# Optimization experiments

Measured on AMD Instinct MI355X. Metric: run time of the kernel, lower is better.

## Reference

```python
import jax, jax.numpy as jnp
import numpy as np

N_NODES = 100000

def _gcn_norm(edge_index, num_nodes):
    # add self-loops, compute symmetric normalization coeffs per edge
    loops = jnp.arange(num_nodes, dtype=edge_index.dtype)
    src = jnp.concatenate([edge_index[0], loops])
    dst = jnp.concatenate([edge_index[1], loops])
    deg = jax.ops.segment_sum(jnp.ones_like(dst, dtype=jnp.float32), dst,
                              num_segments=num_nodes)
    dinv = jnp.where(deg > 0, jax.lax.rsqrt(deg), 0.0)
    norm = dinv[src] * dinv[dst]  # [E + N]
    return src, dst, norm

def _gcn_conv(x, W, b, src, dst, norm, num_nodes):
    h = x @ W                              # [N, out] transform first (PyG order)
    msg = h[src] * norm[:, None]           # gather + scale
    out = jax.ops.segment_sum(msg, dst, num_segments=num_nodes)  # scatter-add
    return out + b

def setup_inputs() -> dict:
    key = jax.random.key(0)
    k1, k2, k3, k4 = jax.random.split(key, 4)
    F_in, H, C = 128, 64, 40
    x = jax.random.normal(k1, (N_NODES, F_in), dtype=jnp.float32)
    edge_index = jax.random.randint(k2, (2, 1600000), 0, N_NODES, dtype=jnp.int64)
    W1 = jax.random.normal(k3, (F_in, H), dtype=jnp.float32) / np.sqrt(F_in)
    b1 = jnp.zeros((H,), dtype=jnp.float32)
    W2 = jax.random.normal(k4, (H, C), dtype=jnp.float32) / np.sqrt(H)
    b2 = jnp.zeros((C,), dtype=jnp.float32)
    return {"x": x, "edge_index": edge_index, "W1": W1, "b1": b1, "W2": W2, "b2": b2}

def reference(x, edge_index, W1, b1, W2, b2):
    num_nodes = x.shape[0]
    src, dst, norm = _gcn_norm(edge_index, num_nodes)
    h = _gcn_conv(x, W1, b1, src, dst, norm, num_nodes)
    h = jax.nn.relu(h)
    # dropout is identity in eval mode (training=False)
    h = _gcn_conv(h, W2, b2, src, dst, norm, num_nodes)
    return jax.nn.log_softmax(h, axis=1)
```

## Files before the change

kernel.cpp:

```cpp
#include <hip/hip_runtime.h>
#include <math.h>

#define NPB 256
#define BSH 8
#define MAXNB 400
#define BIN_CHUNK 8192
#define HIST_CHUNK 16384

typedef __attribute__((ext_vector_type(8))) short bf16x8;
typedef __attribute__((ext_vector_type(4))) float f32x4;
typedef __attribute__((ext_vector_type(2))) float f32x2;

__device__ __forceinline__ unsigned short f2bf(float f){
  unsigned int u = __float_as_uint(f);
  unsigned int r = (u + 0x7FFFu + ((u >> 16) & 1u)) >> 16;
  return (unsigned short)r;
}
__device__ __forceinline__ float bf2f(unsigned int b){
  return __uint_as_float(b << 16);
}

__device__ __forceinline__ bf16x8 cvt8(float4 a, float4 b){
  union { unsigned u[4]; bf16x8 v; } r;
  asm("v_cvt_pk_bf16_f32 %0, %1, %2" : "=v"(r.u[0]) : "v"(a.x), "v"(a.y));
  asm("v_cvt_pk_bf16_f32 %0, %1, %2" : "=v"(r.u[1]) : "v"(a.z), "v"(a.w));
  asm("v_cvt_pk_bf16_f32 %0, %1, %2" : "=v"(r.u[2]) : "v"(b.x), "v"(b.y));
  asm("v_cvt_pk_bf16_f32 %0, %1, %2" : "=v"(r.u[3]) : "v"(b.z), "v"(b.w));
  return r.v;
}


__global__ void k_zero(int* __restrict__ p, int n){
  int i = blockIdx.x*256 + threadIdx.x;
  if(i < n) p[i] = 0;
}

__global__ __launch_bounds__(256) void k_bhist(const int* __restrict__ dst, int E,
                                               int* __restrict__ bcnt, int NB){
  __shared__ int l[MAXNB];
  int t = threadIdx.x;
  int base = blockIdx.x*HIST_CHUNK;
  int end = base + HIST_CHUNK; if(end > E) end = E;
  for(int b = t; b < NB; b += 256) l[b] = 0;
  __syncthreads();
  for(int i = base + t; i < end; i += 256) atomicAdd(&l[dst[i] >> BSH], 1);
  __syncthreads();
  for(int b = t; b < NB; b += 256){ int c = l[b]; if(c) atomicAdd(&bcnt[b], c); }
}

__global__ void k_bscan(const int* __restrict__ bcnt, int* __restrict__ bofs,
                        int* __restrict__ bcur, int NB, int E){
  __shared__ int sh[1024];
  int t = threadIdx.x;
  int c0 = (2*t   < NB) ? bcnt[2*t]   : 0;
  int c1 = (2*t+1 < NB) ? bcnt[2*t+1] : 0;
  sh[t] = c0 + c1; __syncthreads();
  for(int off = 1; off < 1024; off <<= 1){
    int v = (t >= off) ? sh[t - off] : 0;
    __syncthreads();
    sh[t] += v;
    __syncthreads();
  }
  int pairEx = sh[t] - (c0 + c1);
  if(2*t   < NB){ bofs[2*t]   = pairEx;      bcur[2*t]   = pairEx; }
  if(2*t+1 < NB){ bofs[2*t+1] = pairEx + c0; bcur[2*t+1] = pairEx + c0; }
  if(t == 0) bofs[NB] = E;
}

__global__ __launch_bounds__(256) void k_binpass(const int* __restrict__ src,
                          const int* __restrict__ dst, int E,
                          int* __restrict__ bcur, unsigned int* __restrict__ binned, int NB){
  __shared__ int lcnt[MAXNB];
  __shared__ int lpos[MAXNB];
  int t = threadIdx.x;
  int base = blockIdx.x * BIN_CHUNK;
  int end = base + BIN_CHUNK; if(end > E) end = E;
  for(int b = t; b < NB; b += 256) lcnt[b] = 0;
  __syncthreads();
  for(int i = base + t; i < end; i += 256)
    atomicAdd(&lcnt[dst[i] >> BSH], 1);
  __syncthreads();
  for(int b = t; b < NB; b += 256){
    int c = lcnt[b];
    lpos[b] = c ? atomicAdd(&bcur[b], c) : 0;
  }
  __syncthreads();
  for(int i = base + t; i < end; i += 256){
    int d = dst[i];
    int b = d >> BSH;
    unsigned int rec = (unsigned int)src[i] | ((unsigned int)(d & (NPB-1)) << 17);
    int p = atomicAdd(&lpos[b], 1);
    binned[p] = rec;
  }
}

__global__ __launch_bounds__(256) void k_bscatter(const unsigned int* __restrict__ binned,
     const int* __restrict__ bofs, int* __restrict__ csr, int* __restrict__ row_ofs,
     float* __restrict__ dinv, int N, int E, int NB){
  __shared__ int lcnt[NPB];
  __shared__ int lofs[NPB];
  __shared__ int lcur[NPB];
  __shared__ int wsum[4];
  int b = blockIdx.x, t = threadIdx.x;
  int beg = bofs[b], end = bofs[b+1];
  lcnt[t] = 0;
  __syncthreads();
  for(int i = beg + t; i < end; i += 256) atomicAdd(&lcnt[binned[i] >> 17], 1);
  __syncthreads();
  int c = lcnt[t];
  int lane = t & 63, wid = t >> 6;
  int v = c;
  #pragma unroll
  for(int off = 1; off < 64; off <<= 1){
    int nv = __shfl_up(v, off, 64);
    if(lane >= off) v += nv;
  }
  if(lane == 63) wsum[wid] = v;
  __syncthreads();
  int wpre = 0;
  #pragma unroll
  for(int k2 = 0; k2 < 4; k2++) if(k2 < wid) wpre += wsum[k2];
  int ex = wpre + v - c;
  lofs[t] = beg + ex; lcur[t] = 0;
  int node = (b << BSH) + t;
  if(node < N){
    row_ofs[node] = beg + ex;
    dinv[node] = rsqrtf((float)(c + 1));
  }
  __syncthreads();
  for(int i = beg + t; i < end; i += 256){
    unsigned int rec = binned[i];
    int dl = rec >> 17;
    int pos = lofs[dl] + atomicAdd(&lcur[dl], 1);
    csr[pos] = (int)(rec & 0x1FFFFu);
  }
  if(b == NB-1 && t == 0) row_ofs[N] = E;
}

__global__ void k_wprep(const float* __restrict__ W1, unsigned short* __restrict__ w1t){
  int t = threadIdx.x;
  for(int i = t; i < 8192; i += 256){
    int k = i >> 6, f = i & 63;
    w1t[f*128 + k] = f2bf(W1[i]);
  }
}

__global__ __launch_bounds__(256) void k_gemm1(const float* __restrict__ x,
                        const unsigned short* __restrict__ w1t,
                        const float* __restrict__ dinv, unsigned int* __restrict__ g1, int n){
  __shared__ unsigned short wt[64*136];
  int tid = threadIdx.x;
  int nodeBase = blockIdx.x*128;
  for(int i = tid; i < 1024; i += 256){
    int f = i >> 4, seg = i & 15;
    uint4 v = *(const uint4*)&w1t[f*128 + seg*8];
    *(uint4*)&wt[f*136 + seg*8] = v;
  }
  __syncthreads();

  int w = tid >> 6, lane = tid & 63;
  int ml = lane & 15, q = lane >> 4;
  int n0 = nodeBase + w*32 + ml;
  int n1 = n0 + 16;
  bool vn0 = n0 < n, vn1 = n1 < n;
  const float* px0 = x + (size_t)n0*128 + q*8;
  const float* px1 = x + (size_t)n1*128 + q*8;
  const float4 z4 = make_float4(0.f,0.f,0.f,0.f);

  f32x4 a00 = {0.f,0.f,0.f,0.f}, a01 = {0.f,0.f,0.f,0.f},
        a02 = {0.f,0.f,0.f,0.f}, a03 = {0.f,0.f,0.f,0.f};
  f32x4 a10 = {0.f,0.f,0.f,0.f}, a11 = {0.f,0.f,0.f,0.f},
        a12 = {0.f,0.f,0.f,0.f}, a13 = {0.f,0.f,0.f,0.f};
  const unsigned short* arow = &wt[ml*136 + q*8];
  #pragma unroll
  for(int s = 0; s < 4; s++){
    float4 xa0 = vn0 ? *(const float4*)(px0 + s*32)     : z4;
    float4 xb0 = vn0 ? *(const float4*)(px0 + s*32 + 4) : z4;
    float4 xa1 = vn1 ? *(const float4*)(px1 + s*32)     : z4;
    float4 xb1 = vn1 ? *(const float4*)(px1 + s*32 + 4) : z4;
    bf16x8 bb0 = cvt8(xa0, xb0);
    bf16x8 bb1 = cvt8(xa1, xb1);
    bf16x8 a0 = *(const bf16x8*)(arow +    0 + s*32);
    bf16x8 a1 = *(const bf16x8*)(arow + 2176 + s*32);
    bf16x8 a2 = *(const bf16x8*)(arow + 4352 + s*32);
    bf16x8 a3 = *(const bf16x8*)(arow + 6528 + s*32);
    a00 = __builtin_amdgcn_mfma_f32_16x16x32_bf16(a0, bb0, a00, 0, 0, 0);
    a01 = __builtin_amdgcn_mfma_f32_16x16x32_bf16(a1, bb0, a01, 0, 0, 0);
    a02 = __builtin_amdgcn_mfma_f32_16x16x32_bf16(a2, bb0, a02, 0, 0, 0);
    a03 = __builtin_amdgcn_mfma_f32_16x16x32_bf16(a3, bb0, a03, 0, 0, 0);
    a10 = __builtin_amdgcn_mfma_f32_16x16x32_bf16(a0, bb1, a10, 0, 0, 0);
    a11 = __builtin_amdgcn_mfma_f32_16x16x32_bf16(a1, bb1, a11, 0, 0, 0);
    a12 = __builtin_amdgcn_mfma_f32_16x16x32_bf16(a2, bb1, a12, 0, 0, 0);
    a13 = __builtin_amdgcn_mfma_f32_16x16x32_bf16(a3, bb1, a13, 0, 0, 0);
  }
  if(vn0){
    float dv = dinv[n0];
    unsigned base16 = ((unsigned)n0 << 4) + q;
    int p;
    p = __builtin_amdgcn_cvt_pk_fp8_f32(a00[0]*dv, a00[1]*dv, 0, false);
    p = __builtin_amdgcn_cvt_pk_fp8_f32(a00[2]*dv, a00[3]*dv, p, true);
    g1[base16 +  0] = (unsigned)p;
    p = __builtin_amdgcn_cvt_pk_fp8_f32(a01[0]*dv, a01[1]*dv, 0, false);
    p = __builtin_amdgcn_cvt_pk_fp8_f32(a01[2]*dv, a01[3]*dv, p, true);
    g1[base16 +  4] = (unsigned)p;
    p = __builtin_amdgcn_cvt_pk_fp8_f32(a02[0]*dv, a02[1]*dv, 0, false);
    p = __builtin_amdgcn_cvt_pk_fp8_f32(a02[2]*dv, a02[3]*dv, p, true);
    g1[base16 +  8] = (unsigned)p;
    p = __builtin_amdgcn_cvt_pk_fp8_f32(a03[0]*dv, a03[1]*dv, 0, false);
    p = __builtin_amdgcn_cvt_pk_fp8_f32(a03[2]*dv, a03[3]*dv, p, true);
    g1[base16 + 12] = (unsigned)p;
  }
  if(vn1){
    float dv = dinv[n1];
    unsigned base16 = ((unsigned)n1 << 4) + q;
    int p;
    p = __builtin_amdgcn_cvt_pk_fp8_f32(a10[0]*dv, a10[1]*dv, 0, false);
    p = __builtin_amdgcn_cvt_pk_fp8_f32(a10[2]*dv, a10[3]*dv, p, true);
    g1[base16 +  0] = (unsigned)p;
    p = __builtin_amdgcn_cvt_pk_fp8_f32(a11[0]*dv, a11[1]*dv, 0, false);
    p = __builtin_amdgcn_cvt_pk_fp8_f32(a11[2]*dv, a11[3]*dv, p, true);
    g1[base16 +  4] = (unsigned)p;
    p = __builtin_amdgcn_cvt_pk_fp8_f32(a12[0]*dv, a12[1]*dv, 0, false);
    p = __builtin_amdgcn_cvt_pk_fp8_f32(a12[2]*dv, a12[3]*dv, p, true);
    g1[base16 +  8] = (unsigned)p;
    p = __builtin_amdgcn_cvt_pk_fp8_f32(a13[0]*dv, a13[1]*dv, 0, false);
    p = __builtin_amdgcn_cvt_pk_fp8_f32(a13[2]*dv, a13[3]*dv, p, true);
    g1[base16 + 12] = (unsigned)p;
  }
}

__global__ __launch_bounds__(256) void k_agg1(const unsigned* __restrict__ g1,
    const int* __restrict__ row_ofs, const int* __restrict__ csr,
    const float* __restrict__ dinv, const float* __restrict__ b1,
    unsigned short* __restrict__ u, int N){
  int t = threadIdx.x;
  int lane = t & 63;
  int f = lane & 15;
  int bq = (lane & 48) << 2;
  int node = blockIdx.x*16 + (t >> 4);
  if(node >= N) return;
  int beg = row_ofs[node], end = row_ofs[node+1];
  unsigned v = g1[((unsigned)node << 4) + f];
  f32x2 s01 = __builtin_amdgcn_cvt_pk_f32_fp8(v, false);
  f32x2 s23 = __builtin_amdgcn_cvt_pk_f32_fp8(v, true);
  for(int e = beg; e < end; e += 16){
    int rem = end - e; if(rem > 16) rem = 16;
    int idxv = (f < rem) ? csr[e + f] : 0;
    int j = 0;
    for(; j + 4 <= rem; j += 4){
      int r0 = __builtin_amdgcn_ds_bpermute(bq + ((j+0) << 2), idxv);
      int r1 = __builtin_amdgcn_ds_bpermute(bq + ((j+1) << 2), idxv);
      int r2 = __builtin_amdgcn_ds_bpermute(bq + ((j+2) << 2), idxv);
      int r3 = __builtin_amdgcn_ds_bpermute(bq + ((j+3) << 2), idxv);
      unsigned v0 = g1[((unsigned)r0 << 4) + f];
      unsigned v1 = g1[((unsigned)r1 << 4) + f];
      unsigned v2 = g1[((unsigned)r2 << 4) + f];
      unsigned v3 = g1[((unsigned)r3 << 4) + f];
      s01 += __builtin_amdgcn_cvt_pk_f32_fp8(v0, false);
      s23 += __builtin_amdgcn_cvt_pk_f32_fp8(v0, true);
      s01 += __builtin_amdgcn_cvt_pk_f32_fp8(v1, false);
      s23 += __builtin_amdgcn_cvt_pk_f32_fp8(v1, true);
      s01 += __builtin_amdgcn_cvt_pk_f32_fp8(v2, false);
      s23 += __builtin_amdgcn_cvt_pk_f32_fp8(v2, true);
      s01 += __builtin_amdgcn_cvt_pk_f32_fp8(v3, false);
      s23 += __builtin_amdgcn_cvt_pk_f32_fp8(v3, true);
    }
    for(; j < rem; j++){
      int r0 = __builtin_amdgcn_ds_bpermute(bq + (j << 2), idxv);
      unsigned v0 = g1[((unsigned)r0 << 4) + f];
      s01 += __builtin_amdgcn_cvt_pk_f32_fp8(v0, false);
      s23 += __builtin_amdgcn_cvt_pk_f32_fp8(v0, true);
    }
  }
  float dv = dinv[node];
  float4 bb = ((const float4*)b1)[f];
  float h0 = fmaxf(fmaf(dv, s01.x, bb.x), 0.f);
  float h1 = fmaxf(fmaf(dv, s01.y, bb.y), 0.f);
  float h2 = fmaxf(fmaf(dv, s23.x, bb.z), 0.f);
  float h3 = fmaxf(fmaf(dv, s23.y, bb.w), 0.f);
  unsigned p0 = (unsigned)f2bf(dv*h0) | ((unsigned)f2bf(dv*h1) << 16);
  unsigned p1 = (unsigned)f2bf(dv*h2) | ((unsigned)f2bf(dv*h3) << 16);
  ((uint2*)u)[((unsigned)node << 4) + f] = make_uint2(p0, p1);
}

__global__ __launch_bounds__(320) void k_gemm2(const unsigned short* __restrict__ u,
                        const float* __restrict__ W2, unsigned char* __restrict__ g2, int n){
  __shared__ float hs[64*65];
  __shared__ float ws[64*40];
  int t = threadIdx.x;
  int nodeBase = blockIdx.x*64;
  for(int i = t; i < 2560; i += 320) ws[i] = W2[i];
  for(int i = t; i < 512; i += 320){
    int row = i >> 3, seg = i & 7;
    uint4 v = make_uint4(0,0,0,0);
    if(nodeBase + row < n) v = *(const uint4*)&u[(size_t)(nodeBase + row)*64 + seg*8];
    float* dp = &hs[row*65 + seg*8];
    dp[0]=bf2f(v.x&0xFFFFu); dp[1]=bf2f(v.x>>16);
    dp[2]=bf2f(v.y&0xFFFFu); dp[3]=bf2f(v.y>>16);
    dp[4]=bf2f(v.z&0xFFFFu); dp[5]=bf2f(v.z>>16);
    dp[6]=bf2f(v.w&0xFFFFu); dp[7]=bf2f(v.w>>16);
  }
  __syncthreads();
  int seg = t >> 6, lane = t & 63;
  float acc[8] = {0.f,0.f,0.f,0.f,0.f,0.f,0.f,0.f};
  const float* hrow = &hs[lane*65];
  const float* wcol = &ws[seg*8];
  #pragma unroll 4
  for(int k = 0; k < 64; k++){
    float a = hrow[k];
    #pragma unroll
    for(int j = 0; j < 8; j++) acc[j] = fmaf(a, wcol[k*40 + j], acc[j]);
  }
  int node = nodeBase + lane;
  if(node < n){
    int p0 = __builtin_amdgcn_cvt_pk_fp8_f32(acc[0], acc[1], 0, false);
    p0     = __builtin_amdgcn_cvt_pk_fp8_f32(acc[2], acc[3], p0, true);
    int p1 = __builtin_amdgcn_cvt_pk_fp8_f32(acc[4], acc[5], 0, false);
    p1     = __builtin_amdgcn_cvt_pk_fp8_f32(acc[6], acc[7], p1, true);
    *(uint2*)&g2[(size_t)node*40 + seg*8] = make_uint2((unsigned)p0, (unsigned)p1);
  }
}

__global__ __launch_bounds__(256) void k_agg2(const unsigned char* __restrict__ g2,
     const int* __restrict__ row_ofs, const int* __restrict__ csr,
     const float* __restrict__ dinv, const float* __restrict__ b2,
     float* __restrict__ out, int N){
  int t = threadIdx.x;
  int lane = t & 63;
  int f = lane & 15;
  int fc = (f < 10) ? f : 0;
  int bq = (lane & 48) << 2;
  int node = blockIdx.x*16 + (t >> 4);
  if(node >= N) return;
  int beg = row_ofs[node], end = row_ofs[node+1];
  const unsigned* gd = (const unsigned*)g2;
  unsigned v = gd[(unsigned)node*10u + fc];
  f32x2 s01 = __builtin_amdgcn_cvt_pk_f32_fp8(v, false);
  f32x2 s23 = __builtin_amdgcn_cvt_pk_f32_fp8(v, true);
  for(int e = beg; e < end; e += 16){
    int rem = end - e; if(rem > 16) rem = 16;
    int idxv = (f < rem) ? csr[e + f] : 0;
    int j = 0;
    for(; j + 4 <= rem; j += 4){
      int r0 = __builtin_amdgcn_ds_bpermute(bq + ((j+0) << 2), idxv);
      int r1 = __builtin_amdgcn_ds_bpermute(bq + ((j+1) << 2), idxv);
      int r2 = __builtin_amdgcn_ds_bpermute(bq + ((j+2) << 2), idxv);
      int r3 = __builtin_amdgcn_ds_bpermute(bq + ((j+3) << 2), idxv);
      unsigned v0 = gd[(unsigned)r0*10u + fc];
      unsigned v1 = gd[(unsigned)r1*10u + fc];
      unsigned v2 = gd[(unsigned)r2*10u + fc];
      unsigned v3 = gd[(unsigned)r3*10u + fc];
      s01 += __builtin_amdgcn_cvt_pk_f32_fp8(v0, false);
      s23 += __builtin_amdgcn_cvt_pk_f32_fp8(v0, true);
      s01 += __builtin_amdgcn_cvt_pk_f32_fp8(v1, false);
      s23 += __builtin_amdgcn_cvt_pk_f32_fp8(v1, true);
      s01 += __builtin_amdgcn_cvt_pk_f32_fp8(v2, false);
      s23 += __builtin_amdgcn_cvt_pk_f32_fp8(v2, true);
      s01 += __builtin_amdgcn_cvt_pk_f32_fp8(v3, false);
      s23 += __builtin_amdgcn_cvt_pk_f32_fp8(v3, true);
    }
    for(; j < rem; j++){
      int r0 = __builtin_amdgcn_ds_bpermute(bq + (j << 2), idxv);
      unsigned v0 = gd[(unsigned)r0*10u + fc];
      s01 += __builtin_amdgcn_cvt_pk_f32_fp8(v0, false);
      s23 += __builtin_amdgcn_cvt_pk_f32_fp8(v0, true);
    }
  }
  float dv = dinv[node];
  float4 bb = ((const float4*)b2)[fc];
  float l0 = fmaf(dv, s01.x, bb.x);
  float l1 = fmaf(dv, s01.y, bb.y);
  float l2 = fmaf(dv, s23.x, bb.z);
  float l3 = fmaf(dv, s23.y, bb.w);
  bool valid = (f < 10);
  float m = valid ? fmaxf(fmaxf(l0,l1), fmaxf(l2,l3)) : -INFINITY;
  m = fmaxf(m, __shfl_xor(m,1,64)); m = fmaxf(m, __shfl_xor(m,2,64));
  m = fmaxf(m, __shfl_xor(m,4,64)); m = fmaxf(m, __shfl_xor(m,8,64));
  float ex = valid ? (expf(l0-m)+expf(l1-m)) + (expf(l2-m)+expf(l3-m)) : 0.f;
  ex += __shfl_xor(ex,1,64); ex += __shfl_xor(ex,2,64);
  ex += __shfl_xor(ex,4,64); ex += __shfl_xor(ex,8,64);
  float ll = logf(ex);
  if(valid){
    ((float4*)out)[(unsigned)node*10u + f] = make_float4(l0-m-ll, l1-m-ll, l2-m-ll, l3-m-ll);
  }
}


extern "C" void kernel_launch(void* const* d_in, const int* in_sizes, int n_in,
                              void* d_out, int out_size, void* d_ws, size_t ws_size,
                              hipStream_t stream){
  const float* x  = (const float*)d_in[0];
  const int*   ei = (const int*)  d_in[1];
  const float* W1 = (const float*)d_in[2];
  const float* b1 = (const float*)d_in[3];
  const float* W2 = (const float*)d_in[4];
  const float* b2 = (const float*)d_in[5];
  float* out = (float*)d_out;

  int N = in_sizes[0] / 128;
  int E = in_sizes[1] / 2;
  const int* src = ei;
  const int* dst = ei + E;
  int NB = (N + NPB - 1) >> BSH;

  char* w = (char*)d_ws;
  auto alloc = [&](size_t bytes) -> char* {
    char* p = w;
    w += (bytes + 511) & ~(size_t)511;
    return p;
  };
  int*   bcnt    = (int*)  alloc((size_t)NB*4);
  int*   bofs    = (int*)  alloc((size_t)(NB+1)*4);
  int*   bcur    = (int*)  alloc((size_t)NB*4);
  int*   row_ofs = (int*)  alloc((size_t)(N+1)*4);
  float* dinv    = (float*)alloc((size_t)N*4);
  unsigned int* binned = (unsigned int*)alloc((size_t)E*4);
  int*   csr     = (int*)  alloc((size_t)E*4);
  unsigned int*   g1 = (unsigned int*)  alloc((size_t)N*64);
  unsigned short* u  = (unsigned short*)alloc((size_t)N*64*2);
  unsigned char*  g2 = (unsigned char*) alloc((size_t)N*40);
  unsigned short* w1t = (unsigned short*)alloc((size_t)64*128*2);

  k_wprep   <<<1, 256, 0, stream>>>(W1, w1t);
  k_zero    <<<(NB+255)/256, 256, 0, stream>>>(bcnt, NB);
  k_bhist   <<<(E+HIST_CHUNK-1)/HIST_CHUNK, 256, 0, stream>>>(dst, E, bcnt, NB);
  k_bscan   <<<1, 1024, 0, stream>>>(bcnt, bofs, bcur, NB, E);
  k_binpass <<<(E+BIN_CHUNK-1)/BIN_CHUNK, 256, 0, stream>>>(src, dst, E, bcur, binned, NB);
  k_bscatter<<<NB, 256, 0, stream>>>(binned, bofs, csr, row_ofs, dinv, N, E, NB);

  k_gemm1   <<<(N+127)/128, 256, 0, stream>>>(x, w1t, dinv, g1, N);
  k_agg1    <<<(N+15)/16, 256, 0, stream>>>(g1, row_ofs, csr, dinv, b1, u, N);
  k_gemm2   <<<(N+63)/64, 320, 0, stream>>>(u, W2, g2, N);
  k_agg2    <<<(N+15)/16, 256, 0, stream>>>(g2, row_ofs, csr, dinv, b2, out, N);
}
```

Baseline: 261.5 us.

## Use MFMA for second GEMM, stage x tile in LDS, merge prep kernels

```diff
diff --git a/kernel.cpp b/kernel.cpp
--- a/kernel.cpp
+++ b/kernel.cpp
@@ -15,9 +15,6 @@
   unsigned int u = __float_as_uint(f);
   unsigned int r = (u + 0x7FFFu + ((u >> 16) & 1u)) >> 16;
   return (unsigned short)r;
-}
-__device__ __forceinline__ float bf2f(unsigned int b){
-  return __uint_as_float(b << 16);
 }
 
 __device__ __forceinline__ bf16x8 cvt8(float4 a, float4 b){
@@ -29,11 +26,24 @@
   return r.v;
 }
 
-
-__global__ void k_zero(int* __restrict__ p, int n){
-  int i = blockIdx.x*256 + threadIdx.x;
-  if(i < n) p[i] = 0;
-}
+__global__ void k_prep(const float* __restrict__ W1, const float* __restrict__ W2,
+                       unsigned short* __restrict__ w1t, unsigned short* __restrict__ w2t,
+                       int* __restrict__ bcnt, int NB){
+  int t = threadIdx.x;
+  if(blockIdx.x == 0){
+    for(int i = t; i < 8192; i += 256){
+      int k = i >> 6, f = i & 63;
+      w1t[f*128 + k] = f2bf(W1[i]);
+    }
+  } else {
+    for(int i = t; i < 3072; i += 256){
+      int c = i >> 6, k = i & 63;
+      w2t[c*64 + k] = (c < 40) ? f2bf(W2[k*40 + c]) : (unsigned short)0;
+    }
+    for(int i = t; i < NB; i += 256) bcnt[i] = 0;
+  }
+}
+
 
 __global__ __launch_bounds__(256) void k_bhist(const int* __restrict__ dst, int E,
                                                int* __restrict__ bcnt, int NB){
@@ -137,24 +147,28 @@
   if(b == NB-1 && t == 0) row_ofs[N] = E;
 }
 
-__global__ void k_wprep(const float* __restrict__ W1, unsigned short* __restrict__ w1t){
-  int t = threadIdx.x;
-  for(int i = t; i < 8192; i += 256){
-    int k = i >> 6, f = i & 63;
-    w1t[f*128 + k] = f2bf(W1[i]);
-  }
-}
-
 __global__ __launch_bounds__(256) void k_gemm1(const float* __restrict__ x,
                         const unsigned short* __restrict__ w1t,
                         const float* __restrict__ dinv, unsigned int* __restrict__ g1, int n){
+  __shared__ unsigned short xs[128*136];
   __shared__ unsigned short wt[64*136];
   int tid = threadIdx.x;
   int nodeBase = blockIdx.x*128;
   for(int i = tid; i < 1024; i += 256){
     int f = i >> 4, seg = i & 15;
-    uint4 v = *(const uint4*)&w1t[f*128 + seg*8];
-    *(uint4*)&wt[f*136 + seg*8] = v;
+    *(uint4*)&wt[f*136 + seg*8] = *(const uint4*)&w1t[f*128 + seg*8];
+  }
+  {
+    const float4* x4 = (const float4*)x;
+    for(int i = tid; i < 2048; i += 256){
+      int node = i >> 4, seg = i & 15;
+      float4 va = make_float4(0.f,0.f,0.f,0.f), vb = va;
+      if(nodeBase + node < n){
+        va = x4[(size_t)(nodeBase + node)*32 + seg*2];
+        vb = x4[(size_t)(nodeBase + node)*32 + seg*2 + 1];
+      }
+      *(bf16x8*)&xs[node*136 + seg*8] = cvt8(va, vb);
+    }
   }
   __syncthreads();
 
@@ -163,23 +177,17 @@
   int n0 = nodeBase + w*32 + ml;
   int n1 = n0 + 16;
   bool vn0 = n0 < n, vn1 = n1 < n;
-  const float* px0 = x + (size_t)n0*128 + q*8;
-  const float* px1 = x + (size_t)n1*128 + q*8;
-  const float4 z4 = make_float4(0.f,0.f,0.f,0.f);
 
   f32x4 a00 = {0.f,0.f,0.f,0.f}, a01 = {0.f,0.f,0.f,0.f},
         a02 = {0.f,0.f,0.f,0.f}, a03 = {0.f,0.f,0.f,0.f};
   f32x4 a10 = {0.f,0.f,0.f,0.f}, a11 = {0.f,0.f,0.f,0.f},
         a12 = {0.f,0.f,0.f,0.f}, a13 = {0.f,0.f,0.f,0.f};
+  const unsigned short* brow = &xs[(w*32 + ml)*136 + q*8];
   const unsigned short* arow = &wt[ml*136 + q*8];
   #pragma unroll
   for(int s = 0; s < 4; s++){
-    float4 xa0 = vn0 ? *(const float4*)(px0 + s*32)     : z4;
-    float4 xb0 = vn0 ? *(const float4*)(px0 + s*32 + 4) : z4;
-    float4 xa1 = vn1 ? *(const float4*)(px1 + s*32)     : z4;
-    float4 xb1 = vn1 ? *(const float4*)(px1 + s*32 + 4) : z4;
-    bf16x8 bb0 = cvt8(xa0, xb0);
-    bf16x8 bb1 = cvt8(xa1, xb1);
+    bf16x8 bb0 = *(const bf16x8*)(brow +        s*32);
+    bf16x8 bb1 = *(const bf16x8*)(brow + 2176 + s*32);
     bf16x8 a0 = *(const bf16x8*)(arow +    0 + s*32);
     bf16x8 a1 = *(const bf16x8*)(arow + 2176 + s*32);
     bf16x8 a2 = *(const bf16x8*)(arow + 4352 + s*32);
@@ -283,41 +291,55 @@
   ((uint2*)u)[((unsigned)node << 4) + f] = make_uint2(p0, p1);
 }
 
-__global__ __launch_bounds__(320) void k_gemm2(const unsigned short* __restrict__ u,
-                        const float* __restrict__ W2, unsigned char* __restrict__ g2, int n){
-  __shared__ float hs[64*65];
-  __shared__ float ws[64*40];
+__global__ __launch_bounds__(256) void k_gemm2(const unsigned short* __restrict__ u,
+                        const unsigned short* __restrict__ w2t,
+                        unsigned char* __restrict__ g2, int n){
+  __shared__ unsigned short us[64*72];
+  __shared__ unsigned short ws2[48*72];
   int t = threadIdx.x;
   int nodeBase = blockIdx.x*64;
-  for(int i = t; i < 2560; i += 320) ws[i] = W2[i];
-  for(int i = t; i < 512; i += 320){
+  for(int i = t; i < 512; i += 256){
     int row = i >> 3, seg = i & 7;
     uint4 v = make_uint4(0,0,0,0);
     if(nodeBase + row < n) v = *(const uint4*)&u[(size_t)(nodeBase + row)*64 + seg*8];
-    float* dp = &hs[row*65 + seg*8];
-    dp[0]=bf2f(v.x&0xFFFFu); dp[1]=bf2f(v.x>>16);
-    dp[2]=bf2f(v.y&0xFFFFu); dp[3]=bf2f(v.y>>16);
-    dp[4]=bf2f(v.z&0xFFFFu); dp[5]=bf2f(v.z>>16);
-    dp[6]=bf2f(v.w&0xFFFFu); dp[7]=bf2f(v.w>>16);
-  }
-  __syncthreads();
-  int seg = t >> 6, lane = t & 63;
-  float acc[8] = {0.f,0.f,0.f,0.f,0.f,0.f,0.f,0.f};
-  const float* hrow = &hs[lane*65];
-  const float* wcol = &ws[seg*8];
-  #pragma unroll 4
-  for(int k = 0; k < 64; k++){
-    float a = hrow[k];
-    #pragma unroll
-    for(int j = 0; j < 8; j++) acc[j] = fmaf(a, wcol[k*40 + j], acc[j]);
-  }
-  int node = nodeBase + lane;
+    *(uint4*)&us[row*72 + seg*8] = v;
+  }
+  for(int i = t; i < 384; i += 256){
+    int row = i >> 3, seg = i & 7;
+    *(uint4*)&ws2[row*72 + seg*8] = *(const uint4*)&w2t[row*64 + seg*8];
+  }
+  __syncthreads();
+  int w = t >> 6, lane = t & 63;
+  int ml = lane & 15, q = lane >> 4;
+  f32x4 acc0 = {0.f,0.f,0.f,0.f}, acc1 = {0.f,0.f,0.f,0.f}, acc2 = {0.f,0.f,0.f,0.f};
+  const unsigned short* brow = &us[(w*16 + ml)*72 + q*8];
+  const unsigned short* a0r = &ws2[ml*72 + q*8];
+  #pragma unroll
+  for(int s = 0; s < 2; s++){
+    bf16x8 bb = *(const bf16x8*)(brow + s*32);
+    bf16x8 a0 = *(const bf16x8*)(a0r +    0 + s*32);
+    bf16x8 a1 = *(const bf16x8*)(a0r + 1152 + s*32);
+    bf16x8 a2 = *(const bf16x8*)(a0r + 2304 + s*32);
+    acc0 = __builtin_amdgcn_mfma_f32_16x16x32_bf16(a0, bb, acc0, 0, 0, 0);
+    acc1 = __builtin_amdgcn_mfma_f32_16x16x32_bf16(a1, bb, acc1, 0, 0, 0);
+    acc2 = __builtin_amdgcn_mfma_f32_16x16x32_bf16(a2, bb, acc2, 0, 0, 0);
+  }
+  int node = nodeBase + w*16 + ml;
   if(node < n){
-    int p0 = __builtin_amdgcn_cvt_pk_fp8_f32(acc[0], acc[1], 0, false);
-    p0     = __builtin_amdgcn_cvt_pk_fp8_f32(acc[2], acc[3], p0, true);
-    int p1 = __builtin_amdgcn_cvt_pk_fp8_f32(acc[4], acc[5], 0, false);
-    p1     = __builtin_amdgcn_cvt_pk_fp8_f32(acc[6], acc[7], p1, true);
-    *(uint2*)&g2[(size_t)node*40 + seg*8] = make_uint2((unsigned)p0, (unsigned)p1);
+    unsigned* gd = (unsigned*)g2;
+    unsigned rb = (unsigned)node*10u + q;
+    int p;
+    p = __builtin_amdgcn_cvt_pk_fp8_f32(acc0[0], acc0[1], 0, false);
+    p = __builtin_amdgcn_cvt_pk_fp8_f32(acc0[2], acc0[3], p, true);
+    gd[rb + 0] = (unsigned)p;
+    p = __builtin_amdgcn_cvt_pk_fp8_f32(acc1[0], acc1[1], 0, false);
+    p = __builtin_amdgcn_cvt_pk_fp8_f32(acc1[2], acc1[3], p, true);
+    gd[rb + 4] = (unsigned)p;
+    if(q < 2){
+      p = __builtin_amdgcn_cvt_pk_fp8_f32(acc2[0], acc2[1], 0, false);
+      p = __builtin_amdgcn_cvt_pk_fp8_f32(acc2[2], acc2[3], p, true);
+      gd[rb + 8] = (unsigned)p;
+    }
   }
 }
 
@@ -420,9 +442,9 @@
   unsigned short* u  = (unsigned short*)alloc((size_t)N*64*2);
   unsigned char*  g2 = (unsigned char*) alloc((size_t)N*40);
   unsigned short* w1t = (unsigned short*)alloc((size_t)64*128*2);
-
-  k_wprep   <<<1, 256, 0, stream>>>(W1, w1t);
-  k_zero    <<<(NB+255)/256, 256, 0, stream>>>(bcnt, NB);
+  unsigned short* w2t = (unsigned short*)alloc((size_t)48*64*2);
+
+  k_prep    <<<2, 256, 0, stream>>>(W1, W2, w1t, w2t, bcnt, NB);
   k_bhist   <<<(E+HIST_CHUNK-1)/HIST_CHUNK, 256, 0, stream>>>(dst, E, bcnt, NB);
   k_bscan   <<<1, 1024, 0, stream>>>(bcnt, bofs, bcur, NB, E);
   k_binpass <<<(E+BIN_CHUNK-1)/BIN_CHUNK, 256, 0, stream>>>(src, dst, E, bcur, binned, NB);
@@ -430,6 +452,6 @@
 
   k_gemm1   <<<(N+127)/128, 256, 0, stream>>>(x, w1t, dinv, g1, N);
   k_agg1    <<<(N+15)/16, 256, 0, stream>>>(g1, row_ofs, csr, dinv, b1, u, N);
-  k_gemm2   <<<(N+63)/64, 320, 0, stream>>>(u, W2, g2, N);
+  k_gemm2   <<<(N+63)/64, 256, 0, stream>>>(u, w2t, g2, N);
   k_agg2    <<<(N+15)/16, 256, 0, stream>>>(g2, row_ofs, csr, dinv, b2, out, N);
 }
```

Result: faster. 232.3 us (-11.2%).
